# Performance work log

Measured on AMD Instinct MI355X. Metric: run time of the kernel, lower is better.

## Reference

```python
import jax, jax.numpy as jnp
import numpy as np

B, S, D, H, L, V, F = 4, 2048, 512, 8, 4, 32000, 512
EPS = 1e-3  # keras BatchNormalization default epsilon


def setup_inputs() -> dict:
    key = jax.random.key(0)
    ks = jax.random.split(key, 32)
    n = lambda k, shp, sc=0.02: (jax.random.normal(k, shp, jnp.float32) * sc)
    inp = {
        "sequence": jax.random.randint(ks[0], (B, S), 0, V, dtype=jnp.int32),
        # padding mask: 1 for kept tokens, 0 for padded; broadcast over [B,h,S,S]
        "padding_mask": (jax.random.uniform(ks[1], (B, 1, 1, S)) > 0.1).astype(jnp.float32),
        "pos_embeddings": n(ks[2], (S, D), 1.0),
        "emb": n(ks[3], (V, D), 1.0),
        "wq": n(ks[4], (L, D, D)), "bq": jnp.zeros((L, D), jnp.float32),
        "wk": n(ks[5], (L, D, D)), "bk": jnp.zeros((L, D), jnp.float32),
        "wv": n(ks[6], (L, D, D)), "bv": jnp.zeros((L, D), jnp.float32),
        "wo": n(ks[7], (L, D, D)), "bo": jnp.zeros((L, D), jnp.float32),
        "an_gamma": 1.0 + n(ks[8], (L, D)), "an_beta": n(ks[9], (L, D)),
        "an_mean": n(ks[10], (L, D), 0.1), "an_var": 0.5 + jax.random.uniform(ks[11], (L, D)),
        "d1_w": n(ks[12], (L, D, F)), "d1_b": jnp.zeros((L, F), jnp.float32),
        "d2_w": n(ks[13], (L, F, D)), "d2_b": jnp.zeros((L, D), jnp.float32),
        "fn_gamma": 1.0 + n(ks[14], (L, D)), "fn_beta": n(ks[15], (L, D)),
        "fn_mean": n(ks[16], (L, D), 0.1), "fn_var": 0.5 + jax.random.uniform(ks[17], (L, D)),
    }
    return inp


def _bn(x, gamma, beta, mean, var):
    # keras BatchNormalization in inference mode (moving statistics), axis=-1
    return (x - mean) * jax.lax.rsqrt(var + EPS) * gamma + beta


def reference(sequence, padding_mask, pos_embeddings, emb,
              wq, bq, wk, bk, wv, bv, wo, bo,
              an_gamma, an_beta, an_mean, an_var,
              d1_w, d1_b, d2_w, d2_b,
              fn_gamma, fn_beta, fn_mean, fn_var):
    b, s = sequence.shape
    nlayers, d, _ = wq.shape
    h = H
    dk = d // h
    scale = 1.0 / jnp.sqrt(jnp.float32(dk))

    x = emb[sequence] + pos_embeddings[:s, :]  # [B,S,D]

    def split_heads(t):  # [B,S,D] -> [B,h,S,dk]
        return t.reshape(b, s, h, dk).transpose(0, 2, 1, 3)

    for i in range(nlayers):
        q = split_heads(x @ wq[i] + bq[i])
        k = split_heads(x @ wk[i] + bk[i])
        v = split_heads(x @ wv[i] + bv[i])
        score = jnp.einsum('bhqd,bhkd->bhqk', q, k) * scale  # [B,h,S,S]
        if padding_mask is not None:
            score = score * padding_mask
            score = jnp.where(score == 0, jnp.float32(-1e9), score)
        align = jax.nn.softmax(score, axis=-1)
        ctx = jnp.einsum('bhqk,bhkd->bhqd', align, v)
        ctx = ctx.transpose(0, 2, 1, 3).reshape(b, s, d)
        heads = ctx @ wo[i] + bo[i]
        sub = _bn(x + heads, an_gamma[i], an_beta[i], an_mean[i], an_var[i])
        ffn = jax.nn.relu(sub @ d1_w[i] + d1_b[i]) @ d2_w[i] + d2_b[i]
        x = _bn(sub + ffn, fn_gamma[i], fn_beta[i], fn_mean[i], fn_var[i])
    return x
```

## Files before the change

### kernel.cpp

```cpp
#include <hip/hip_runtime.h>
#include <stdint.h>
#include <stddef.h>

constexpr int BB = 4, SS = 2048, DD = 512, HH = 8, LL = 4;
constexpr int NTOK = BB * SS;
constexpr float BN_EPS = 1e-3f;

using bh = __bf16;
typedef __bf16 bf16x8 __attribute__((ext_vector_type(8)));
typedef float  f32x4  __attribute__((ext_vector_type(4)));

#define DEV __device__ __forceinline__
#define WAITVM(n) asm volatile("s_waitcnt vmcnt(" #n ")" ::: "memory")
#define WAITLGKM0 asm volatile("s_waitcnt lgkmcnt(0)" ::: "memory")

DEV void gload_lds16(const void* g, void* l) {
    __builtin_amdgcn_global_load_lds(
        (const __attribute__((address_space(1))) void*)g,
        (__attribute__((address_space(3))) void*)l, 16, 0, 0);
}

__global__ void wprep(const float* __restrict__ in, bh* __restrict__ out, int ostride) {
    __shared__ float t[32][33];
    const float* ip = in + (size_t)blockIdx.z * DD * DD;
    bh* op = out + (size_t)blockIdx.z * ostride;
    const int r0 = blockIdx.y * 32, c0 = blockIdx.x * 32;
    const int tx = threadIdx.x, ty = threadIdx.y;
    #pragma unroll
    for (int i = ty; i < 32; i += 8) t[i][tx] = ip[(size_t)(r0 + i) * DD + c0 + tx];
    __syncthreads();
    #pragma unroll
    for (int i = ty; i < 32; i += 8) op[(size_t)(c0 + i) * DD + r0 + tx] = (bh)t[tx][i];
}

__global__ void maskprep(const float* __restrict__ mask, float* __restrict__ mb) {
    const int i = ((int)blockIdx.x * 256 + threadIdx.x) * 4;
    const float4 m4 = *(const float4*)(mask + i);
    float4 o;
    o.x = (m4.x == 0.f) ? -1e30f : 0.f;
    o.y = (m4.y == 0.f) ? -1e30f : 0.f;
    o.z = (m4.z == 0.f) ? -1e30f : 0.f;
    o.w = (m4.w == 0.f) ? -1e30f : 0.f;
    *(float4*)(mb + i) = o;
}

__global__ void embed_k(const int* __restrict__ seq, const float* __restrict__ emb,
                        const float* __restrict__ pos, bh* __restrict__ xb) {
    const int m = blockIdx.x;
    const int s = m & (SS - 1);
    const int tok = seq[m];
    const int d = threadIdx.x * 4;
    const float4 e  = *(const float4*)(emb + (size_t)tok * DD + d);
    const float4 pz = *(const float4*)(pos + (size_t)s * DD + d);
    union { bh h[4]; uint64_t u; } pk;
    pk.h[0] = (bh)(e.x + pz.x); pk.h[1] = (bh)(e.y + pz.y);
    pk.h[2] = (bh)(e.z + pz.z); pk.h[3] = (bh)(e.w + pz.w);
    *(uint64_t*)(xb + (size_t)m * DD + d) = pk.u;
}

template <int EP, bool WF32>
__global__ __launch_bounds__(256, 4)
void gemm64(const bh* __restrict__ A, const bh* __restrict__ Bt,
            const float* __restrict__ bias, bh* __restrict__ outb,
            const bh* __restrict__ resb, float* __restrict__ Xo,
            const float* __restrict__ gamma, const float* __restrict__ beta,
            const float* __restrict__ mean, const float* __restrict__ var) {
    constexpr int BK = 64, NKT = DD / BK;
    __shared__ __align__(16) bh As[2][64 * BK];
    __shared__ __align__(16) bh Bs[2][64 * BK];

    const int tid = threadIdx.x;
    const int w = tid >> 6, lane = tid & 63;
    const int l15 = lane & 15, l4 = lane >> 4;
    const int i = (int)blockIdx.x;
    const int xcd = i & 7, j = i >> 3;
    const int bm = xcd * 16 + (j >> 3);
    const int bn = j & 7;
    const int m0 = bm * 64, n0 = bn * 64;
    const int wr = w >> 1, wc = w & 1;

    f32x4 acc[2][2] = {};
    const int sr = lane >> 3;
    const int cbx = (lane & 7) ^ sr;

    auto stage = [&](int buf, int kk) {
        #pragma unroll
        for (int ii = 0; ii < 2; ++ii) {
            const int idx = w * 2 + ii;
            const int r = idx * 8 + sr;
            gload_lds16(A + (size_t)(m0 + r) * DD + kk + 8 * cbx, &As[buf][idx * 512]);
            gload_lds16(Bt + (size_t)(n0 + r) * DD + kk + 8 * cbx, &Bs[buf][idx * 512]);
        }
    };

    stage(0, 0);
    __syncthreads();

    for (int kt = 0; kt < NKT; ++kt) {
        const int buf = kt & 1;
        if (kt > 0) { WAITVM(0); __builtin_amdgcn_s_barrier(); }
        if (kt + 1 < NKT) stage(buf ^ 1, (kt + 1) * BK);

        const char* Ab = (const char*)&As[buf][0];
        const char* Bb = (const char*)&Bs[buf][0];
        #pragma unroll
        for (int ks = 0; ks < 2; ++ks) {
            bf16x8 af[2], bfr[2];
            const int cby = ks * 64 + l4 * 16;
            #pragma unroll
            for (int mf = 0; mf < 2; ++mf) {
                const int row = wr * 32 + mf * 16 + l15;
                af[mf] = *(const bf16x8*)(Ab + row * 128 + (cby ^ ((row & 7) << 4)));
            }
            #pragma unroll
            for (int nf = 0; nf < 2; ++nf) {
                const int row = wc * 32 + nf * 16 + l15;
                bfr[nf] = *(const bf16x8*)(Bb + row * 128 + (cby ^ ((row & 7) << 4)));
            }
            __builtin_amdgcn_s_setprio(1);
            #pragma unroll
            for (int mf = 0; mf < 2; ++mf)
                #pragma unroll
                for (int nf = 0; nf < 2; ++nf)
                    acc[mf][nf] = __builtin_amdgcn_mfma_f32_16x16x32_bf16(
                        af[mf], bfr[nf], acc[mf][nf], 0, 0, 0);
            __builtin_amdgcn_s_setprio(0);
        }
    }

    #pragma unroll
    for (int nf = 0; nf < 2; ++nf) {
        const int n = n0 + wc * 32 + nf * 16 + l15;
        const float bi = bias[n];
        float g = 0.f, be = 0.f, mu = 0.f, iv = 0.f;
        if constexpr (EP == 1) {
            g = gamma[n]; be = beta[n]; mu = mean[n];
            iv = rsqrtf(var[n] + BN_EPS);
        }
        #pragma unroll
        for (int mf = 0; mf < 2; ++mf) {
            #pragma unroll
            for (int r = 0; r < 4; ++r) {
                const int m = m0 + wr * 32 + mf * 16 + l4 * 4 + r;
                const size_t off = (size_t)m * DD + n;
                const float v = acc[mf][nf][r] + bi;
                if constexpr (EP == 2) {
                    outb[off] = (bh)fmaxf(v, 0.f);
                } else {
                    const float t = (float)resb[off] + v;
                    const float s = (t - mu) * iv * g + be;
                    outb[off] = (bh)s;
                    if constexpr (WF32) Xo[off] = s;
                }
            }
        }
    }
}

__global__ __launch_bounds__(256, 3)
void gemm_qkv(const bh* __restrict__ A, const bh* __restrict__ Bt,
              const float* __restrict__ bq, const float* __restrict__ bk,
              const float* __restrict__ bv,
              bh* __restrict__ qb, bh* __restrict__ kb, bh* __restrict__ vT) {
    constexpr int BM = 128, BN = 64, BK = 64, NKT = DD / BK;
    __shared__ __align__(16) bh As[2][BM * BK];
    __shared__ __align__(16) bh Bs[2][BN * BK];

    const int tid = threadIdx.x;
    const int w = tid >> 6, lane = tid & 63;
    const int l15 = lane & 15, l4 = lane >> 4;
    const int i = (int)blockIdx.x;
    const int xcd = i & 7, j = i >> 3;
    const int bm = xcd * 8 + (j & 7);
    const int bn = j >> 3;
    const int m0 = bm * BM, n0 = bn * BN;
    const int wr = w >> 1, wc = w & 1;

    f32x4 acc[4][2] = {};
    const int sr = lane >> 3;
    const int cbx = (lane & 7) ^ sr;

    auto stage = [&](int buf, int kk) {
        #pragma unroll
        for (int ii = 0; ii < 4; ++ii) {
            const int idx = w * 4 + ii;
            const int r = idx * 8 + sr;
            gload_lds16(A + (size_t)(m0 + r) * DD + kk + 8 * cbx, &As[buf][idx * 512]);
        }
        #pragma unroll
        for (int ii = 0; ii < 2; ++ii) {
            const int idx = w * 2 + ii;
            const int r = idx * 8 + sr;
            gload_lds16(Bt + (size_t)(n0 + r) * DD + kk + 8 * cbx, &Bs[buf][idx * 512]);
        }
    };

    stage(0, 0);
    stage(1, BK);

    for (int kt = 0; kt < NKT; ++kt) {
        const int buf = kt & 1;
        if (kt + 1 < NKT) { WAITVM(6); } else { WAITVM(0); }
        __builtin_amdgcn_s_barrier();

        const char* Ab = (const char*)&As[buf][0];
        const char* Bb = (const char*)&Bs[buf][0];
        #pragma unroll
        for (int ks = 0; ks < 2; ++ks) {
            bf16x8 af[4], bfr[2];
            const int cby = ks * 64 + l4 * 16;
            #pragma unroll
            for (int mf = 0; mf < 4; ++mf) {
                const int row = wr * 64 + mf * 16 + l15;
                af[mf] = *(const bf16x8*)(Ab + row * 128 + (cby ^ ((row & 7) << 4)));
            }
            #pragma unroll
            for (int nf = 0; nf < 2; ++nf) {
                const int row = wc * 32 + nf * 16 + l15;
                bfr[nf] = *(const bf16x8*)(Bb + row * 128 + (cby ^ ((row & 7) << 4)));
            }
            #pragma unroll
            for (int mf = 0; mf < 4; ++mf)
                #pragma unroll
                for (int nf = 0; nf < 2; ++nf)
                    acc[mf][nf] = __builtin_amdgcn_mfma_f32_16x16x32_bf16(
                        af[mf], bfr[nf], acc[mf][nf], 0, 0, 0);
        }
        WAITLGKM0;
        __builtin_amdgcn_s_barrier();
        if (kt + 2 < NKT) stage(buf, (kt + 2) * BK);
    }

    const int part = n0 >> 9;
    #pragma unroll
    for (int nf = 0; nf < 2; ++nf) {
        const int n = n0 + wc * 32 + nf * 16 + l15;
        const int nn = n & 511;
        const float bi = (part == 0 ? bq : part == 1 ? bk : bv)[nn];
        if (part < 2) {
            bh* out = part ? kb : qb;
            #pragma unroll
            for (int mf = 0; mf < 4; ++mf)
                #pragma unroll
                for (int r = 0; r < 4; ++r) {
                    const int m = m0 + wr * 64 + mf * 16 + l4 * 4 + r;
                    out[(size_t)m * DD + nn] = (bh)(acc[mf][nf][r] + bi);
                }
        } else {
            const int hh = nn >> 6, dk = nn & 63;
            #pragma unroll
            for (int mf = 0; mf < 4; ++mf) {
                const int m = m0 + wr * 64 + mf * 16 + l4 * 4;
                const int bb2 = m >> 11, s = m & (SS - 1);
                union { bh h4[4]; uint64_t u; } pk;
                #pragma unroll
                for (int r = 0; r < 4; ++r)
                    pk.h4[r] = (bh)(acc[mf][nf][r] + bi);
                *(uint64_t*)(vT + ((size_t)((bb2 * HH + hh) * 64) + dk) * SS + s) = pk.u;
            }
        }
    }
}

__global__ __launch_bounds__(256, 4)
void flash_attn(const bh* __restrict__ Q, const bh* __restrict__ K,
                const bh* __restrict__ VT, const float* __restrict__ mb,
                bh* __restrict__ O) {
    constexpr int KVB = 32, NT = SS / KVB;
    constexpr float CSC = 0.18033688f;
    __shared__ __align__(16) bh Ks[2][KVB * 64];
    __shared__ __align__(16) bh Vs[2][64 * KVB];
    __shared__ __align__(16) bh Plds[4][16 * 40];

    const int tid = threadIdx.x;
    const int w = tid >> 6, lane = tid & 63;
    const int l15 = lane & 15, l4 = lane >> 4;

    const int i = (int)blockIdx.x;
    const int xcd = i & 7, j = i >> 3;
    const int g = xcd * 4 + (j >> 5);
    const int qt = j & 31;
    const int h = g & 7, b = g >> 3;

    const int q0 = qt * 64 + w * 16;

    const bh* qp = Q + (size_t)(b * SS + q0 + l15) * DD + h * 64 + l4 * 8;
    const bf16x8 qf0 = *(const bf16x8*)qp;
    const bf16x8 qf1 = *(const bf16x8*)(qp + 32);

    f32x4 ctx[4] = {};
    f32x4 accl = {};
    float m2 = -3e38f;

    bf16x8 ones;
    #pragma unroll
    for (int z = 0; z < 8; ++z) ones[z] = (bh)1.0f;

    const int ksr = lane >> 3;
    const int kcb = (lane & 7) ^ ksr;
    const int vrow = lane >> 2;
    const int vcb  = (lane & 3) ^ (vrow & 3);

    const bh* kg = K + ((size_t)(b * SS) + w * 8 + ksr) * DD + h * 64 + 8 * kcb;
    const bh* vg = VT + ((size_t)((b * HH + h) * 64) + w * 16 + vrow) * SS + 8 * vcb;
    const float* mbb = mb + (size_t)b * SS + l4 * 4;

    auto stage = [&](int buf, int kt) {
        gload_lds16(kg + (size_t)kt * DD, &Ks[buf][w * 512]);
        gload_lds16(vg + kt,              &Vs[buf][w * 512]);
    };

    f32x4 mbc[2];
    stage(0, 0);
    mbc[0] = *(const f32x4*)(mbb);
    mbc[1] = *(const f32x4*)(mbb + 16);
    __syncthreads();

    for (int t = 0; t < NT; ++t) {
        const int buf = t & 1;
        const int kt = t * KVB;
        if (t > 0) { WAITVM(2); __builtin_amdgcn_s_barrier(); }
        if (t + 1 < NT) stage(buf ^ 1, kt + KVB);

        const char* Kb = (const char*)&Ks[buf][0];
        bf16x8 kf[2][2];
        #pragma unroll
        for (int ks = 0; ks < 2; ++ks)
            #pragma unroll
            for (int nf = 0; nf < 2; ++nf) {
                const int row = nf * 16 + l15;
                kf[ks][nf] = *(const bf16x8*)(Kb + row * 128 +
                              ((ks * 64 + l4 * 16) ^ ((row & 7) << 4)));
            }
        f32x4 sc[2] = {};
        __builtin_amdgcn_s_setprio(1);
        #pragma unroll
        for (int ks = 0; ks < 2; ++ks)
            #pragma unroll
            for (int nf = 0; nf < 2; ++nf)
                sc[nf] = __builtin_amdgcn_mfma_f32_16x16x32_bf16(
                    kf[ks][nf], ks ? qf1 : qf0, sc[nf], 0, 0, 0);
        __builtin_amdgcn_s_setprio(0);

        float tm = -3e38f;
        #pragma unroll
        for (int nf = 0; nf < 2; ++nf)
            #pragma unroll
            for (int r = 0; r < 4; ++r) {
                const float z = fmaf(sc[nf][r], CSC, mbc[nf][r]);
                sc[nf][r] = z;
                tm = fmaxf(tm, z);
            }
        if (__any(tm > m2 + 11.5f)) {
            tm = fmaxf(tm, __shfl_xor(tm, 16, 64));
            tm = fmaxf(tm, __shfl_xor(tm, 32, 64));
            const float mn = fmaxf(fmaxf(tm, m2), -60.f);
            const float fac = __builtin_amdgcn_exp2f(m2 - mn);
            m2 = mn;
            accl *= fac;
            #pragma unroll
            for (int nf = 0; nf < 4; ++nf)
                #pragma unroll
                for (int r = 0; r < 4; ++r)
                    ctx[nf][r] *= fac;
        }

        char* Pw = (char*)&Plds[w][0] + l15 * 80;
        #pragma unroll
        for (int nf = 0; nf < 2; ++nf) {
            union { bh h4[4]; uint64_t u; } pk;
            #pragma unroll
            for (int r = 0; r < 4; ++r)
                pk.h4[r] = (bh)__builtin_amdgcn_exp2f(sc[nf][r] - m2);
            *(uint64_t*)(Pw + nf * 32 + l4 * 8) = pk.u;
        }
        WAITLGKM0;
        const bf16x8 pa = *(const bf16x8*)(Pw + l4 * 16);

        const char* Vb = (const char*)&Vs[buf][0];
        bf16x8 vf[4];
        #pragma unroll
        for (int nf = 0; nf < 4; ++nf) {
            const int row = nf * 16 + l15;
            vf[nf] = *(const bf16x8*)(Vb + row * 64 + ((l4 ^ (l15 & 3)) << 4));
        }
        __builtin_amdgcn_s_setprio(1);
        #pragma unroll
        for (int nf = 0; nf < 4; ++nf)
            ctx[nf] = __builtin_amdgcn_mfma_f32_16x16x32_bf16(vf[nf], pa, ctx[nf], 0, 0, 0);
        accl = __builtin_amdgcn_mfma_f32_16x16x32_bf16(ones, pa, accl, 0, 0, 0);
        __builtin_amdgcn_s_setprio(0);

        if (t + 1 < NT) {
            mbc[0] = *(const f32x4*)(mbb + kt + KVB);
            mbc[1] = *(const f32x4*)(mbb + kt + KVB + 16);
        }
    }

    const float linv = 1.0f / accl[0];
    #pragma unroll
    for (int nf = 0; nf < 4; ++nf) {
        union { bh h4[4]; uint64_t u; } pk;
        #pragma unroll
        for (int r = 0; r < 4; ++r)
            pk.h4[r] = (bh)(ctx[nf][r] * linv);
        *(uint64_t*)(O + (size_t)(b * SS + q0 + l15) * DD +
                     h * 64 + nf * 16 + l4 * 4) = pk.u;
    }
}

extern "C" void kernel_launch(void* const* d_in, const int* in_sizes, int n_in,
                              void* d_out, int out_size, void* d_ws, size_t ws_size,
                              hipStream_t stream) {
    const int*   seq  = (const int*)  d_in[0];
    const float* mask = (const float*)d_in[1];
    const float* pos  = (const float*)d_in[2];
    const float* emb  = (const float*)d_in[3];
    const float* wq = (const float*)d_in[4];  const float* bq = (const float*)d_in[5];
    const float* wk = (const float*)d_in[6];  const float* bk = (const float*)d_in[7];
    const float* wv = (const float*)d_in[8];  const float* bv = (const float*)d_in[9];
    const float* wo = (const float*)d_in[10]; const float* bo = (const float*)d_in[11];
    const float* ag = (const float*)d_in[12]; const float* ab = (const float*)d_in[13];
    const float* am = (const float*)d_in[14]; const float* av = (const float*)d_in[15];
    const float* d1w = (const float*)d_in[16]; const float* d1b = (const float*)d_in[17];
    const float* d2w = (const float*)d_in[18]; const float* d2b = (const float*)d_in[19];
    const float* fg = (const float*)d_in[20]; const float* fb = (const float*)d_in[21];
    const float* fm = (const float*)d_in[22]; const float* fv = (const float*)d_in[23];

    float* X = (float*)d_out;

    char* p = (char*)d_ws;
    auto take = [&](size_t n) { char* q = p; p += (n + 255) & ~(size_t)255; return q; };
    const size_t WE  = (size_t)LL * DD * DD;
    const size_t WQE = (size_t)LL * 3 * DD * DD;
    bh* wcat = (bh*)take(WQE * 2);
    bh* wot = (bh*)take(WE * 2);
    bh* w1t = (bh*)take(WE * 2);
    bh* w2t = (bh*)take(WE * 2);
    const size_t AE = (size_t)NTOK * DD;
    bh* xb   = (bh*)take(AE * 2);
    bh* qb   = (bh*)take(AE * 2);
    bh* kb   = (bh*)take(AE * 2);
    bh* ctxb = (bh*)take(AE * 2);
    bh* subb = (bh*)take(AE * 2);
    bh* h1b  = (bh*)take(AE * 2);
    bh* vT   = (bh*)take(AE * 2);
    float* mbias = (float*)take((size_t)BB * SS * 4);

    const int QKV_OS = 3 * DD * DD;
    const dim3 wg(16, 16, LL), wb(32, 8);
    wprep<<<wg, wb, 0, stream>>>(wq,  wcat + 0 * DD * DD, QKV_OS);
    wprep<<<wg, wb, 0, stream>>>(wk,  wcat + 1 * DD * DD, QKV_OS);
    wprep<<<wg, wb, 0, stream>>>(wv,  wcat + 2 * DD * DD, QKV_OS);
    wprep<<<wg, wb, 0, stream>>>(wo,  wot, DD * DD);
    wprep<<<wg, wb, 0, stream>>>(d1w, w1t, DD * DD);
    wprep<<<wg, wb, 0, stream>>>(d2w, w2t, DD * DD);

    maskprep<<<dim3(BB * SS / 1024), dim3(256), 0, stream>>>(mask, mbias);
    embed_k<<<dim3(NTOK), dim3(128), 0, stream>>>(seq, emb, pos, xb);

    for (int l = 0; l < LL; ++l) {
        const size_t wof = (size_t)l * DD * DD;
        const int    bof = l * DD;
        gemm_qkv<<<dim3(1536), dim3(256), 0, stream>>>(
            xb, wcat + (size_t)l * QKV_OS, bq + bof, bk + bof, bv + bof, qb, kb, vT);
        flash_attn<<<dim3(1024), dim3(256), 0, stream>>>(qb, kb, vT, mbias, ctxb);
        gemm64<1, false><<<dim3(1024), dim3(256), 0, stream>>>(
            ctxb, wot + wof, bo + bof, subb, xb, nullptr,
            ag + bof, ab + bof, am + bof, av + bof);
        gemm64<2, false><<<dim3(1024), dim3(256), 0, stream>>>(
            subb, w1t + wof, d1b + bof, h1b, nullptr, nullptr,
            nullptr, nullptr, nullptr, nullptr);
        if (l + 1 < LL) {
            gemm64<1, false><<<dim3(1024), dim3(256), 0, stream>>>(
                h1b, w2t + wof, d2b + bof, xb, subb, nullptr,
                fg + bof, fb + bof, fm + bof, fv + bof);
        } else {
            gemm64<1, true><<<dim3(1024), dim3(256), 0, stream>>>(
                h1b, w2t + wof, d2b + bof, xb, subb, X,
                fg + bof, fb + bof, fm + bof, fv + bof);
        }
    }
}
```

Baseline: 467.9 us.

## Pre-swizzle K/V into MFMA fragment layout and rewrite attention with 32x32 MFMA

The QKV GEMM epilogue now writes K and V in a blocked layout that matches the MFMA operand fragments, so flash attention can load them straight into registers with coalesced 16-byte loads. This removes the LDS staging, barriers and the LDS round-trip for P. The attention kernel moves to 128-thread blocks where each wave owns 32 queries and uses 32x32x16 MFMAs, with register double-buffered prefetch and permlane32 swaps to build the P operand. The six weight-prep launches are also merged into one. In exchange, register pressure rises and each wave reloads K/V directly from global/L2 without sharing through LDS.

```diff
diff --git a/kernel.cpp b/kernel.cpp
--- a/kernel.cpp
+++ b/kernel.cpp
@@ -9,6 +9,7 @@
 using bh = __bf16;
 typedef __bf16 bf16x8 __attribute__((ext_vector_type(8)));
 typedef float  f32x4  __attribute__((ext_vector_type(4)));
+typedef float  f32x16 __attribute__((ext_vector_type(16)));
 
 #define DEV __device__ __forceinline__
 #define WAITVM(n) asm volatile("s_waitcnt vmcnt(" #n ")" ::: "memory")
@@ -20,17 +21,33 @@
         (__attribute__((address_space(3))) void*)l, 16, 0, 0);
 }
 
-__global__ void wprep(const float* __restrict__ in, bh* __restrict__ out, int ostride) {
+__global__ void wprep_all(const float* __restrict__ wq, const float* __restrict__ wk,
+                          const float* __restrict__ wv, const float* __restrict__ wo,
+                          const float* __restrict__ d1, const float* __restrict__ d2,
+                          bh* __restrict__ wcat, bh* __restrict__ wot,
+                          bh* __restrict__ w1t, bh* __restrict__ w2t) {
     __shared__ float t[32][33];
-    const float* ip = in + (size_t)blockIdx.z * DD * DD;
-    bh* op = out + (size_t)blockIdx.z * ostride;
+    const int z = blockIdx.z;
+    const int m = z >> 2, l = z & 3;
+    constexpr int QOS = 3 * DD * DD;
+    const float* src;
+    bh* dst;
+    switch (m) {
+        case 0:  src = wq; dst = wcat + (size_t)l * QOS;               break;
+        case 1:  src = wk; dst = wcat + (size_t)l * QOS + DD * DD;     break;
+        case 2:  src = wv; dst = wcat + (size_t)l * QOS + 2 * DD * DD; break;
+        case 3:  src = wo; dst = wot + (size_t)l * DD * DD;            break;
+        case 4:  src = d1; dst = w1t + (size_t)l * DD * DD;            break;
+        default: src = d2; dst = w2t + (size_t)l * DD * DD;            break;
+    }
+    src += (size_t)l * DD * DD;
     const int r0 = blockIdx.y * 32, c0 = blockIdx.x * 32;
     const int tx = threadIdx.x, ty = threadIdx.y;
     #pragma unroll
-    for (int i = ty; i < 32; i += 8) t[i][tx] = ip[(size_t)(r0 + i) * DD + c0 + tx];
+    for (int i = ty; i < 32; i += 8) t[i][tx] = src[(size_t)(r0 + i) * DD + c0 + tx];
     __syncthreads();
     #pragma unroll
-    for (int i = ty; i < 32; i += 8) op[(size_t)(c0 + i) * DD + r0 + tx] = (bh)t[tx][i];
+    for (int i = ty; i < 32; i += 8) dst[(size_t)(c0 + i) * DD + r0 + tx] = (bh)t[tx][i];
 }
 
 __global__ void maskprep(const float* __restrict__ mask, float* __restrict__ mb) {
@@ -161,7 +178,7 @@
 void gemm_qkv(const bh* __restrict__ A, const bh* __restrict__ Bt,
               const float* __restrict__ bq, const float* __restrict__ bk,
               const float* __restrict__ bv,
-              bh* __restrict__ qb, bh* __restrict__ kb, bh* __restrict__ vT) {
+              bh* __restrict__ qb, bh* __restrict__ kblk, bh* __restrict__ vblk) {
     constexpr int BM = 128, BN = 64, BK = 64, NKT = DD / BK;
     __shared__ __align__(16) bh As[2][BM * BK];
     __shared__ __align__(16) bh Bs[2][BN * BK];
@@ -237,175 +254,178 @@
         const int n = n0 + wc * 32 + nf * 16 + l15;
         const int nn = n & 511;
         const float bi = (part == 0 ? bq : part == 1 ? bk : bv)[nn];
-        if (part < 2) {
-            bh* out = part ? kb : qb;
+        if (part == 0) {
             #pragma unroll
             for (int mf = 0; mf < 4; ++mf)
                 #pragma unroll
                 for (int r = 0; r < 4; ++r) {
                     const int m = m0 + wr * 64 + mf * 16 + l4 * 4 + r;
-                    out[(size_t)m * DD + nn] = (bh)(acc[mf][nf][r] + bi);
+                    qb[(size_t)m * DD + nn] = (bh)(acc[mf][nf][r] + bi);
+                }
+        } else if (part == 1) {
+            const int hh = nn >> 6, dk = nn & 63;
+            const int s = dk >> 4, hib = (dk >> 3) & 1, jj = dk & 7;
+            #pragma unroll
+            for (int mf = 0; mf < 4; ++mf)
+                #pragma unroll
+                for (int r = 0; r < 4; ++r) {
+                    const int m = m0 + wr * 64 + mf * 16 + l4 * 4 + r;
+                    const int b2 = m >> 11, sq = m & (SS - 1);
+                    const int tile = sq >> 5, key5 = sq & 31;
+                    kblk[(size_t)(((b2 * HH + hh) * 64 + tile) * 4 + s) * 512 +
+                         (key5 + 32 * hib) * 8 + jj] = (bh)(acc[mf][nf][r] + bi);
                 }
         } else {
             const int hh = nn >> 6, dk = nn & 63;
+            const int half = dk >> 5, lanelow = dk & 31;
             #pragma unroll
             for (int mf = 0; mf < 4; ++mf) {
                 const int m = m0 + wr * 64 + mf * 16 + l4 * 4;
-                const int bb2 = m >> 11, s = m & (SS - 1);
+                const int b2 = m >> 11, sq = m & (SS - 1);
+                const int tile = sq >> 5, key5 = sq & 31;
+                const int ks = key5 >> 4, hib = (key5 >> 3) & 1, jb = key5 & 7;
                 union { bh h4[4]; uint64_t u; } pk;
                 #pragma unroll
                 for (int r = 0; r < 4; ++r)
                     pk.h4[r] = (bh)(acc[mf][nf][r] + bi);
-                *(uint64_t*)(vT + ((size_t)((bb2 * HH + hh) * 64) + dk) * SS + s) = pk.u;
-            }
-        }
-    }
-}
-
-__global__ __launch_bounds__(256, 4)
-void flash_attn(const bh* __restrict__ Q, const bh* __restrict__ K,
-                const bh* __restrict__ VT, const float* __restrict__ mb,
+                *(uint64_t*)(vblk + (size_t)(((b2 * HH + hh) * 64 + tile) * 4 +
+                             half * 2 + ks) * 512 + (lanelow + 32 * hib) * 8 + jb) = pk.u;
+            }
+        }
+    }
+}
+
+__global__ __launch_bounds__(128, 2)
+void flash_attn(const bh* __restrict__ Q, const bh* __restrict__ Kb_,
+                const bh* __restrict__ Vb_, const float* __restrict__ mb,
                 bh* __restrict__ O) {
     constexpr int KVB = 32, NT = SS / KVB;
     constexpr float CSC = 0.18033688f;
-    __shared__ __align__(16) bh Ks[2][KVB * 64];
-    __shared__ __align__(16) bh Vs[2][64 * KVB];
-    __shared__ __align__(16) bh Plds[4][16 * 40];
 
     const int tid = threadIdx.x;
     const int w = tid >> 6, lane = tid & 63;
-    const int l15 = lane & 15, l4 = lane >> 4;
+    const int l31 = lane & 31, hi = lane >> 5;
 
     const int i = (int)blockIdx.x;
     const int xcd = i & 7, j = i >> 3;
     const int g = xcd * 4 + (j >> 5);
     const int qt = j & 31;
     const int h = g & 7, b = g >> 3;
-
-    const int q0 = qt * 64 + w * 16;
-
-    const bh* qp = Q + (size_t)(b * SS + q0 + l15) * DD + h * 64 + l4 * 8;
-    const bf16x8 qf0 = *(const bf16x8*)qp;
-    const bf16x8 qf1 = *(const bf16x8*)(qp + 32);
-
-    f32x4 ctx[4] = {};
-    f32x4 accl = {};
-    float m2 = -3e38f;
-
-    bf16x8 ones;
-    #pragma unroll
-    for (int z = 0; z < 8; ++z) ones[z] = (bh)1.0f;
-
-    const int ksr = lane >> 3;
-    const int kcb = (lane & 7) ^ ksr;
-    const int vrow = lane >> 2;
-    const int vcb  = (lane & 3) ^ (vrow & 3);
-
-    const bh* kg = K + ((size_t)(b * SS) + w * 8 + ksr) * DD + h * 64 + 8 * kcb;
-    const bh* vg = VT + ((size_t)((b * HH + h) * 64) + w * 16 + vrow) * SS + 8 * vcb;
-    const float* mbb = mb + (size_t)b * SS + l4 * 4;
-
-    auto stage = [&](int buf, int kt) {
-        gload_lds16(kg + (size_t)kt * DD, &Ks[buf][w * 512]);
-        gload_lds16(vg + kt,              &Vs[buf][w * 512]);
-    };
-
-    f32x4 mbc[2];
-    stage(0, 0);
-    mbc[0] = *(const f32x4*)(mbb);
-    mbc[1] = *(const f32x4*)(mbb + 16);
-    __syncthreads();
-
-    for (int t = 0; t < NT; ++t) {
-        const int buf = t & 1;
-        const int kt = t * KVB;
-        if (t > 0) { WAITVM(2); __builtin_amdgcn_s_barrier(); }
-        if (t + 1 < NT) stage(buf ^ 1, kt + KVB);
-
-        const char* Kb = (const char*)&Ks[buf][0];
-        bf16x8 kf[2][2];
-        #pragma unroll
-        for (int ks = 0; ks < 2; ++ks)
-            #pragma unroll
-            for (int nf = 0; nf < 2; ++nf) {
-                const int row = nf * 16 + l15;
-                kf[ks][nf] = *(const bf16x8*)(Kb + row * 128 +
-                              ((ks * 64 + l4 * 16) ^ ((row & 7) << 4)));
-            }
-        f32x4 sc[2] = {};
+    const int q0 = qt * 64 + w * 32;
+
+    const bh* qp = Q + (size_t)(b * SS + q0 + l31) * DD + h * 64 + hi * 8;
+    const bf16x8 qf0 = *(const bf16x8*)(qp);
+    const bf16x8 qf1 = *(const bf16x8*)(qp + 16);
+    const bf16x8 qf2 = *(const bf16x8*)(qp + 32);
+    const bf16x8 qf3 = *(const bf16x8*)(qp + 48);
+
+    const bh* kbase = Kb_ + (size_t)((b * HH + h) * 256) * 512 + lane * 8;
+    const bh* vbase = Vb_ + (size_t)((b * HH + h) * 256) * 512 + lane * 8;
+    const float* mbb = mb + (size_t)b * SS + hi * 4;
+
+    f32x16 ctx0 = {}, ctx1 = {};
+    float accl = 0.f, m2 = -3e38f;
+
+    bf16x8 kA0, kA1, kA2, kA3, vA0, vA1, vA2, vA3;
+    bf16x8 kB0, kB1, kB2, kB3, vB0, vB1, vB2, vB3;
+    f32x4 mA0, mA1, mA2, mA3, mB0, mB1, mB2, mB3;
+
+#define PREF(G, t) do {                                                   \
+        const bh* kp_ = kbase + (size_t)(t) * 2048;                       \
+        k##G##0 = *(const bf16x8*)(kp_);                                  \
+        k##G##1 = *(const bf16x8*)(kp_ + 512);                            \
+        k##G##2 = *(const bf16x8*)(kp_ + 1024);                           \
+        k##G##3 = *(const bf16x8*)(kp_ + 1536);                           \
+        const bh* vp_ = vbase + (size_t)(t) * 2048;                       \
+        v##G##0 = *(const bf16x8*)(vp_);                                  \
+        v##G##1 = *(const bf16x8*)(vp_ + 512);                            \
+        v##G##2 = *(const bf16x8*)(vp_ + 1024);                           \
+        v##G##3 = *(const bf16x8*)(vp_ + 1536);                           \
+        const float* mp_ = mbb + (t) * KVB;                               \
+        m##G##0 = *(const f32x4*)(mp_);                                   \
+        m##G##1 = *(const f32x4*)(mp_ + 8);                               \
+        m##G##2 = *(const f32x4*)(mp_ + 16);                              \
+        m##G##3 = *(const f32x4*)(mp_ + 24);                              \
+    } while (0)
+
+    auto compute = [&](const bf16x8& K0, const bf16x8& K1, const bf16x8& K2, const bf16x8& K3,
+                       const bf16x8& V0, const bf16x8& V1, const bf16x8& V2, const bf16x8& V3,
+                       const f32x4& M0, const f32x4& M1, const f32x4& M2, const f32x4& M3) {
+        f32x16 sc = {};
         __builtin_amdgcn_s_setprio(1);
-        #pragma unroll
-        for (int ks = 0; ks < 2; ++ks)
-            #pragma unroll
-            for (int nf = 0; nf < 2; ++nf)
-                sc[nf] = __builtin_amdgcn_mfma_f32_16x16x32_bf16(
-                    kf[ks][nf], ks ? qf1 : qf0, sc[nf], 0, 0, 0);
+        sc = __builtin_amdgcn_mfma_f32_32x32x16_bf16(K0, qf0, sc, 0, 0, 0);
+        sc = __builtin_amdgcn_mfma_f32_32x32x16_bf16(K1, qf1, sc, 0, 0, 0);
+        sc = __builtin_amdgcn_mfma_f32_32x32x16_bf16(K2, qf2, sc, 0, 0, 0);
+        sc = __builtin_amdgcn_mfma_f32_32x32x16_bf16(K3, qf3, sc, 0, 0, 0);
         __builtin_amdgcn_s_setprio(0);
 
+        const f32x4 mm[4] = {M0, M1, M2, M3};
+        float z[16];
         float tm = -3e38f;
         #pragma unroll
-        for (int nf = 0; nf < 2; ++nf)
-            #pragma unroll
-            for (int r = 0; r < 4; ++r) {
-                const float z = fmaf(sc[nf][r], CSC, mbc[nf][r]);
-                sc[nf][r] = z;
-                tm = fmaxf(tm, z);
+        for (int qg = 0; qg < 4; ++qg)
+            #pragma unroll
+            for (int c = 0; c < 4; ++c) {
+                const float zz = fmaf(sc[qg * 4 + c], CSC, mm[qg][c]);
+                z[qg * 4 + c] = zz;
+                tm = fmaxf(tm, zz);
             }
         if (__any(tm > m2 + 11.5f)) {
-            tm = fmaxf(tm, __shfl_xor(tm, 16, 64));
-            tm = fmaxf(tm, __shfl_xor(tm, 32, 64));
-            const float mn = fmaxf(fmaxf(tm, m2), -60.f);
+            const float tp = fmaxf(tm, __shfl_xor(tm, 32, 64));
+            const float mn = fmaxf(fmaxf(tp, m2), -60.f);
             const float fac = __builtin_amdgcn_exp2f(m2 - mn);
             m2 = mn;
             accl *= fac;
             #pragma unroll
-            for (int nf = 0; nf < 4; ++nf)
-                #pragma unroll
-                for (int r = 0; r < 4; ++r)
-                    ctx[nf][r] *= fac;
-        }
-
-        char* Pw = (char*)&Plds[w][0] + l15 * 80;
-        #pragma unroll
-        for (int nf = 0; nf < 2; ++nf) {
-            union { bh h4[4]; uint64_t u; } pk;
-            #pragma unroll
-            for (int r = 0; r < 4; ++r)
-                pk.h4[r] = (bh)__builtin_amdgcn_exp2f(sc[nf][r] - m2);
-            *(uint64_t*)(Pw + nf * 32 + l4 * 8) = pk.u;
-        }
-        WAITLGKM0;
-        const bf16x8 pa = *(const bf16x8*)(Pw + l4 * 16);
-
-        const char* Vb = (const char*)&Vs[buf][0];
-        bf16x8 vf[4];
-        #pragma unroll
-        for (int nf = 0; nf < 4; ++nf) {
-            const int row = nf * 16 + l15;
-            vf[nf] = *(const bf16x8*)(Vb + row * 64 + ((l4 ^ (l15 & 3)) << 4));
-        }
+            for (int r = 0; r < 16; ++r) { ctx0[r] *= fac; ctx1[r] *= fac; }
+        }
+        uint32_t pk[8];
+        float ps = 0.f;
+        #pragma unroll
+        for (int i2 = 0; i2 < 8; ++i2) {
+            const float p0 = __builtin_amdgcn_exp2f(z[2 * i2] - m2);
+            const float p1 = __builtin_amdgcn_exp2f(z[2 * i2 + 1] - m2);
+            ps += p0 + p1;
+            asm("v_cvt_pk_bf16_f32 %0, %1, %2" : "=v"(pk[i2]) : "v"(p0), "v"(p1));
+        }
+        accl += ps;
+        asm("v_permlane32_swap_b32 %0, %1" : "+v"(pk[0]), "+v"(pk[2]));
+        asm("v_permlane32_swap_b32 %0, %1" : "+v"(pk[1]), "+v"(pk[3]));
+        asm("v_permlane32_swap_b32 %0, %1" : "+v"(pk[4]), "+v"(pk[6]));
+        asm("v_permlane32_swap_b32 %0, %1" : "+v"(pk[5]), "+v"(pk[7]));
+        union U { uint32_t d[4]; bf16x8 v; } u0, u1;
+        u0.d[0] = pk[0]; u0.d[1] = pk[1]; u0.d[2] = pk[2]; u0.d[3] = pk[3];
+        u1.d[0] = pk[4]; u1.d[1] = pk[5]; u1.d[2] = pk[6]; u1.d[3] = pk[7];
         __builtin_amdgcn_s_setprio(1);
-        #pragma unroll
-        for (int nf = 0; nf < 4; ++nf)
-            ctx[nf] = __builtin_amdgcn_mfma_f32_16x16x32_bf16(vf[nf], pa, ctx[nf], 0, 0, 0);
-        accl = __builtin_amdgcn_mfma_f32_16x16x32_bf16(ones, pa, accl, 0, 0, 0);
+        ctx0 = __builtin_amdgcn_mfma_f32_32x32x16_bf16(V0, u0.v, ctx0, 0, 0, 0);
+        ctx0 = __builtin_amdgcn_mfma_f32_32x32x16_bf16(V1, u1.v, ctx0, 0, 0, 0);
+        ctx1 = __builtin_amdgcn_mfma_f32_32x32x16_bf16(V2, u0.v, ctx1, 0, 0, 0);
+        ctx1 = __builtin_amdgcn_mfma_f32_32x32x16_bf16(V3, u1.v, ctx1, 0, 0, 0);
         __builtin_amdgcn_s_setprio(0);
-
-        if (t + 1 < NT) {
-            mbc[0] = *(const f32x4*)(mbb + kt + KVB);
-            mbc[1] = *(const f32x4*)(mbb + kt + KVB + 16);
-        }
-    }
-
-    const float linv = 1.0f / accl[0];
+    };
+
+    PREF(A, 0);
+    for (int t = 0; t < NT; t += 2) {
+        PREF(B, t + 1);
+        compute(kA0, kA1, kA2, kA3, vA0, vA1, vA2, vA3, mA0, mA1, mA2, mA3);
+        PREF(A, t + 2);
+        compute(kB0, kB1, kB2, kB3, vB0, vB1, vB2, vB3, mB0, mB1, mB2, mB3);
+    }
+#undef PREF
+
+    const float lr = accl + __shfl_xor(accl, 32, 64);
+    const float linv = 1.0f / lr;
+    bh* op = O + (size_t)(b * SS + q0 + l31) * DD + h * 64 + hi * 4;
     #pragma unroll
-    for (int nf = 0; nf < 4; ++nf) {
-        union { bh h4[4]; uint64_t u; } pk;
-        #pragma unroll
-        for (int r = 0; r < 4; ++r)
-            pk.h4[r] = (bh)(ctx[nf][r] * linv);
-        *(uint64_t*)(O + (size_t)(b * SS + q0 + l15) * DD +
-                     h * 64 + nf * 16 + l4 * 4) = pk.u;
+    for (int rg = 0; rg < 4; ++rg) {
+        union { bh h4[4]; uint64_t u; } pk0, pk1;
+        #pragma unroll
+        for (int r = 0; r < 4; ++r) {
+            pk0.h4[r] = (bh)(ctx0[rg * 4 + r] * linv);
+            pk1.h4[r] = (bh)(ctx1[rg * 4 + r] * linv);
+        }
+        *(uint64_t*)(op + rg * 8) = pk0.u;
+        *(uint64_t*)(op + 32 + rg * 8) = pk1.u;
     }
 }
 
@@ -440,21 +460,17 @@
     const size_t AE = (size_t)NTOK * DD;
     bh* xb   = (bh*)take(AE * 2);
     bh* qb   = (bh*)take(AE * 2);
-    bh* kb   = (bh*)take(AE * 2);
+    bh* kblk = (bh*)take(AE * 2);
+    bh* vblk = (bh*)take(AE * 2);
     bh* ctxb = (bh*)take(AE * 2);
     bh* subb = (bh*)take(AE * 2);
     bh* h1b  = (bh*)take(AE * 2);
-    bh* vT   = (bh*)take(AE * 2);
     float* mbias = (float*)take((size_t)BB * SS * 4);
+    (void)take(16384);
 
     const int QKV_OS = 3 * DD * DD;
-    const dim3 wg(16, 16, LL), wb(32, 8);
-    wprep<<<wg, wb, 0, stream>>>(wq,  wcat + 0 * DD * DD, QKV_OS);
-    wprep<<<wg, wb, 0, stream>>>(wk,  wcat + 1 * DD * DD, QKV_OS);
-    wprep<<<wg, wb, 0, stream>>>(wv,  wcat + 2 * DD * DD, QKV_OS);
-    wprep<<<wg, wb, 0, stream>>>(wo,  wot, DD * DD);
-    wprep<<<wg, wb, 0, stream>>>(d1w, w1t, DD * DD);
-    wprep<<<wg, wb, 0, stream>>>(d2w, w2t, DD * DD);
+    wprep_all<<<dim3(16, 16, 24), dim3(32, 8), 0, stream>>>(
+        wq, wk, wv, wo, d1w, d2w, wcat, wot, w1t, w2t);
 
     maskprep<<<dim3(BB * SS / 1024), dim3(256), 0, stream>>>(mask, mbias);
     embed_k<<<dim3(NTOK), dim3(128), 0, stream>>>(seq, emb, pos, xb);
@@ -463,8 +479,8 @@
         const size_t wof = (size_t)l * DD * DD;
         const int    bof = l * DD;
         gemm_qkv<<<dim3(1536), dim3(256), 0, stream>>>(
-            xb, wcat + (size_t)l * QKV_OS, bq + bof, bk + bof, bv + bof, qb, kb, vT);
-        flash_attn<<<dim3(1024), dim3(256), 0, stream>>>(qb, kb, vT, mbias, ctxb);
+            xb, wcat + (size_t)l * QKV_OS, bq + bof, bk + bof, bv + bof, qb, kblk, vblk);
+        flash_attn<<<dim3(1024), dim3(128), 0, stream>>>(qb, kblk, vblk, mbias, ctxb);
         gemm64<1, false><<<dim3(1024), dim3(256), 0, stream>>>(
             ctxb, wot + wof, bo + bof, subb, xb, nullptr,
             ag + bof, ab + bof, am + bof, av + bof);
```

Result: faster. 432.6 us, median of 5 (-7.5%).
